# Performance work log

Measured on AMD Instinct MI355X. Metric: run time of the kernel, lower is better.

## Reference

```python
import jax, jax.numpy as jnp
import numpy as np

B, C, T_LEN, T_LAT = 32, 512, 1024, 31
T = T_LAT + 1          # t_len_block
NB = T_LEN // T        # n_blocks (t_pad == 0 by construction)
FS_SCALE = 10.0        # FastSigmoid surrogate scale

@jax.custom_vjp
def spike_fs(x):
    return (x > 0).astype(x.dtype)

def _fs_fwd(x):
    return (x > 0).astype(x.dtype), x

def _fs_bwd(x, g):
    return (g / (FS_SCALE * jnp.abs(x) + 1.0) ** 2,)

spike_fs.defvjp(_fs_fwd, _fs_bwd)

def _g(z):
    # keep entries exactly == 1, zero others; gradient passes through identically
    return z - jax.lax.stop_gradient(jnp.where(z == 1.0, 0.0, z))

def setup_inputs() -> dict:
    key = jax.random.key(0)
    k1, k2, k3, k4, k5 = jax.random.split(key, 5)
    x = jax.random.normal(k1, (B, C, T_LEN), jnp.float32)
    beta_raw = jax.random.uniform(k2, (C,), jnp.float32, 0.8, 0.95)   # _beta param
    rec_weight = jnp.eye(C, dtype=jnp.float32) + 0.05 * jax.random.normal(k3, (C, C), jnp.float32)
    p_raw = jax.random.uniform(k4, (C,), jnp.float32, 0.7, 0.95)      # _p param
    b_raw = jax.random.uniform(k5, (C,), jnp.float32, 0.3, 0.7)       # _b param
    return {"x": x, "beta_raw": beta_raw, "rec_weight": rec_weight, "p_raw": p_raw, "b_raw": b_raw}

def _forward(x, beta_raw, rec_weight, p_raw, b_raw):
    dt = x.dtype
    beta = jnp.clip(beta_raw, 0.001, 0.999)
    p = jnp.clip(jnp.abs(p_raw), 0.0, 0.999)
    b = jnp.clip(jnp.abs(b_raw), 0.001, 1.0)

    idx = jnp.arange(T)
    tril = idx[:, None] >= idx[None, :]
    # causal decay kernel: K[c,t,s] = beta_c**(t-s) for s<=t (== bconv1d with beta kernel)
    K = jnp.where(tril[None], beta[:, None, None] ** jnp.maximum(idx[:, None] - idx[None, :], 0).astype(dt), 0.0)
    # phi kernel: z[t] = sum_{s<=t} spikes[s] * (t-s+1)
    Zm = jnp.where(tril, (idx[:, None] - idx[None, :] + 1).astype(dt), 0.0)
    p_pow = p[:, None] ** jnp.arange(1, T + 1, dtype=dt)[None, :]  # (C,T)

    def block(cur, v_init, v_th):
        cur = cur.at[:, :, 0].add(beta[None, :] * v_init)
        mem = jnp.einsum('cts,bcs->bct', K, cur)          # (B,C,T)
        fs = spike_fs(mem - v_th)
        z = jnp.einsum('ts,bcs->bct', Zm, fs)
        return _g(z), z, mem

    Bx = x.shape[0]
    x_blocks = x.reshape(Bx, C, NB, T).transpose(2, 0, 1, 3)  # (NB,B,C,T)

    spikes0, z0, mem0 = block(x_blocks[0], jnp.zeros((Bx, C), dt), jnp.ones((Bx, C, T), dt))
    a_kernel0 = jnp.zeros((Bx, C, T), dt)

    def body(carry, x_slice):
        spikes_prev, z_prev, mem_last, a_kernel = carry
        sp_det = jax.lax.stop_gradient(spikes_prev)          # detach_spike_grad=True
        x_slice = x_slice + jnp.einsum('ij,bjt->bit', rec_weight, sp_det)
        mask_f = (jnp.max(sp_det, axis=2) != 0.0).astype(dt)  # (B,C) spike mask
        x_slice = jnp.where(z_prev < mask_f[:, :, None], 0.0, x_slice)  # refractory suppression
        v_init = mem_last * (1.0 - mask_f)
        # adaptation
        a_at_spike = jnp.sum(a_kernel * sp_det, axis=2) + 1.0 / p[None, :]
        decay_steps = jnp.sum((z_prev > 1.0).astype(dt), axis=2)
        new_a = a_at_spike * p[None, :] ** decay_steps
        a = a_kernel[:, :, -1] * (1.0 - mask_f) + new_a * mask_f
        a_kernel = p_pow[None] * a[:, :, None]               # (B,C,T)
        v_th = 1.0 + b[None, :, None] * a_kernel
        spikes, z, mem = block(x_slice, v_init, v_th)
        return (spikes, z, mem[:, :, -1], a_kernel), spikes

    carry0 = (spikes0, z0, mem0[:, :, -1], a_kernel0)
    _, spikes_rest = jax.lax.scan(body, carry0, x_blocks[1:])
    all_spikes = jnp.concatenate([spikes0[None], spikes_rest], axis=0)  # (NB,B,C,T)
    return all_spikes.transpose(1, 2, 0, 3).reshape(Bx, C, NB * T)

def reference(x, beta_raw, rec_weight, p_raw, b_raw):
    return _forward(x, beta_raw, rec_weight, p_raw, b_raw)
```

## Files before the change

### kernel.cpp

```cpp
#include <hip/hip_runtime.h>
#include <stdint.h>
#include <stddef.h>

#define CH     512
#define TT     32
#define NBLK   32
#define NBATCH 32
#define NCHUNK 8
#define NTHR   1024

__global__ __launch_bounds__(256) void transpose_k(const float* __restrict__ W,
                                                   float* __restrict__ WT) {
    __shared__ float tile[64][65];
    const int bx = blockIdx.x & 7, by = blockIdx.x >> 3;
    const int lx = threadIdx.x & 63, ly = threadIdx.x >> 6;
    for (int r = ly; r < 64; r += 4)
        tile[r][lx] = W[(size_t)(by * 64 + r) * CH + bx * 64 + lx];
    __syncthreads();
    for (int r = ly; r < 64; r += 4)
        WT[(size_t)(bx * 64 + r) * CH + by * 64 + lx] = tile[lx][r];
}

__global__ __launch_bounds__(NTHR, 4) void snn_kernel(
    const float* __restrict__ x,
    const float* __restrict__ beta_raw,
    const float* __restrict__ WT,
    const float* __restrict__ p_raw,
    const float* __restrict__ b_raw,
    int*       __restrict__ ent_g,
    float*     __restrict__ out)
{
    __shared__ float rec8[8][2112];
    __shared__ float rec_tot[2112];
    __shared__ int   ent_lds[512];
    __shared__ int   cnt_lds[8];
    __shared__ int   tf_lds[64];
    __shared__ int   tmp16[64];

    const int bidx = blockIdx.x;
    const int b    = bidx & (NBATCH - 1);
    const int kown = bidx >> 5;
    const int tid  = threadIdx.x;
    const int l    = tid & 63;
    const int g    = tid >> 6;
    const size_t base = ((size_t)b) << 19;
    int* pg = ent_g + (b << 8);

    const int c = (kown << 6) + l;
    const float beta  = fminf(fmaxf(beta_raw[c], 0.001f), 0.999f);
    const float p     = fminf(fabsf(p_raw[c]), 0.999f);
    const float bb    = fminf(fmaxf(fabsf(b_raw[c]), 0.001f), 1.0f);
    const float inv_p = 1.0f / p;
    float p32; { float t2 = p*p, t4 = t2*t2, t8 = t4*t4, t16 = t8*t8; p32 = t16*t16; }
    float a_mult = 0.f, v_init = 0.f;
    int   zero_start = 0;
    const unsigned long long lowmask = (1ull << l) - 1ull;

    if (tid < 512) {
        const int ch = tid >> 3, q = tid & 7;
        const float4 v = *(const float4*)(x + base + ((size_t)((kown << 6) + ch) << 10) + (q << 2));
        float* d = &rec8[0][ch * 33 + (q << 2)];
        d[0] = v.x; d[1] = v.y; d[2] = v.z; d[3] = v.w;
    } else {
        const int t0 = tid - 512;
        #pragma unroll
        for (int z = 0; z < 29; ++z) {
            const int k = t0 + (z << 9);
            if (k < 14784) (&rec8[1][0])[k] = 0.f;
        }
    }
    __syncthreads();

    for (int n = 0; n < NBLK; ++n) {
        int e0 = 0, e1 = 0, sp0 = 0, sp1 = 0;
        if (n > 0) {
            if (tid < 256) {
                const unsigned want = (unsigned)((n - 1) & 15);
                unsigned v;
                while (true) {
                    v = (unsigned)__hip_atomic_load(pg + tid, __ATOMIC_RELAXED, __HIP_MEMORY_SCOPE_AGENT);
                    if ((((v >> 12) & 15u) == want) && (((v >> 28) & 15u) == want)) break;
                    __builtin_amdgcn_s_sleep(1);
                }
                e0 = (int)(v & 0xFFFFu); e1 = (int)((v >> 16) & 0xFFFFu);
                sp0 = ((e0 >> 6) & 63) != 63;
                sp1 = ((e1 >> 6) & 63) != 63;
                const unsigned long long b0 = __ballot(sp0 != 0);
                const unsigned long long b1 = __ballot(sp1 != 0);
                if (l == 0) {
                    cnt_lds[(g << 1)]     = (int)__popcll(b0 & 0xFFFFFFFFull) + (int)__popcll(b1 & 0xFFFFFFFFull);
                    cnt_lds[(g << 1) | 1] = (int)__popcll(b0 >> 32) + (int)__popcll(b1 >> 32);
                }
            } else if (g == 8) {
                #pragma unroll
                for (int it = 0; it < 8; ++it) {
                    const int slot = (it << 6) + l;
                    const int ch = slot >> 3, q = slot & 7;
                    const int tf = tf_lds[ch];
                    const int t0 = q << 2;
                    float4 v;
                    v.x = (t0     == tf) ? 1.f : 0.f;
                    v.y = (t0 + 1 == tf) ? 1.f : 0.f;
                    v.z = (t0 + 2 == tf) ? 1.f : 0.f;
                    v.w = (t0 + 3 == tf) ? 1.f : 0.f;
                    *(float4*)(out + base + ((size_t)((kown << 6) + ch) << 10) + ((n - 1) << 5) + t0) = v;
                }
            }
        }
        __syncthreads();

        int L = 0;
        if (n > 0) {
            int pref = 0;
            const int mychunk = tid >> 5;
            #pragma unroll
            for (int k2 = 0; k2 < 8; ++k2) {
                const int ck = cnt_lds[k2];
                if (k2 < mychunk) pref += ck;
                L += ck;
            }
            if (tid < 256) {
                const int s0 = (tid & 31) << 1;
                const int chbase = (tid >> 5) << 6;
                if (sp0) ent_lds[pref + s0]     = ((chbase | (e0 & 63)) << 5) | ((e0 >> 6) & 31);
                if (sp1) ent_lds[pref + s0 + 1] = ((chbase | (e1 & 63)) << 5) | ((e1 >> 6) & 31);
            }
        }
        __syncthreads();

        float4 xstage;
        if (g >= 8) {
            if (n + 1 < NBLK) {
                const int slot = tid - 512;
                const int ch = slot >> 3, q = slot & 7;
                xstage = *(const float4*)(x + base + ((size_t)((kown << 6) + ch) << 10) + ((n + 1) << 5) + (q << 2));
            }
        } else if (L > 0) {
            const char* WTb = (const char*)WT;
            const int col4 = ((kown << 6) + l) << 2;
            float* myrec = &rec8[g][l * 33];
            float acc = 0.f; int cur_t = -1;
            #pragma unroll
            for (int s = 0; s < 8; ++s) {
                const int segbase = s << 6;
                if (segbase < L) {
                    const int ve = ent_lds[segbase + l];
                    int S[8]; float F[8];
                    #pragma unroll
                    for (int k = 0; k < 8; ++k) {
                        const int idx = segbase + g + (k << 3);
                        int sv = __builtin_amdgcn_readlane(ve, g + (k << 3));
                        const int ok = idx < L;
                        S[k] = ok ? sv : -1;
                        sv = ok ? sv : 0;
                        F[k] = *(const float*)(WTb + ((sv & 0xFFE0) << 6) + col4);
                    }
                    #pragma unroll
                    for (int k = 0; k < 8; ++k) {
                        if (S[k] >= 0) {
                            const int t = S[k] & 31;
                            if (t != cur_t) { if (cur_t >= 0) myrec[cur_t] += acc; acc = 0.f; cur_t = t; }
                            acc += F[k];
                        }
                    }
                }
            }
            if (cur_t >= 0) myrec[cur_t] += acc;
        }
        __syncthreads();

        #pragma unroll
        for (int r = 0; r < 2; ++r) {
            const int e = tid + (r << 10);
            const int idx = ((e >> 5) * 33) + (e & 31);
            rec_tot[idx] = ((rec8[0][idx] + rec8[1][idx]) + (rec8[2][idx] + rec8[3][idx]))
                         + ((rec8[4][idx] + rec8[5][idx]) + (rec8[6][idx] + rec8[7][idx]));
        }
        __syncthreads();

        if (g == 0) {
            float mem = 0.f, pc = p, pca = p;
            int t_first = -1;
            #pragma unroll
            for (int t = 0; t < TT; ++t) {
                const float rv = rec_tot[l * 33 + t];
                float cur = (t >= zero_start) ? rv : 0.f;
                if (t == 0) cur += beta * v_init;
                mem = beta * mem + cur;
                const float vth = 1.f + bb * pc * a_mult;
                if ((mem - vth > 0.f) && t_first < 0) { t_first = t; pca = pc; }
                pc *= p;
            }
            if (t_first >= 0) {
                float pd = 1.f;
                for (int m = 31 - t_first; m > 0; --m) pd *= p;
                a_mult = (pca * a_mult + inv_p) * pd;
                v_init = 0.f; zero_start = t_first;
            } else {
                a_mult = p32 * a_mult;
                v_init = mem; zero_start = 0;
            }
            tf_lds[l] = t_first;
            if (n + 1 < NBLK) {
                const bool sp = (t_first >= 0);
                const unsigned long long balS = __ballot(sp);
                const int cntS = (int)__popcll(balS);
                int mypos;
                if (sp) {
                    unsigned prefc = 0; int mp = 0;
                    #pragma unroll
                    for (int t = 0; t < TT; ++t) {
                        const unsigned long long bal = __ballot(t_first == t);
                        if (t_first == t) mp = (int)prefc + (int)__popcll(bal & lowmask);
                        prefc += (unsigned)__popcll(bal);
                    }
                    mypos = mp;
                } else {
                    mypos = cntS + (int)__popcll(~balS & lowmask);
                }
                const int tval = sp ? t_first : 63;
                tmp16[mypos] = ((n & 15) << 12) | (tval << 6) | l;
                __threadfence_block();
                if (l < 32) {
                    const int wlo = tmp16[l << 1];
                    const int whi = tmp16[(l << 1) | 1];
                    __hip_atomic_store(pg + (kown << 5) + l, wlo | (whi << 16),
                                       __ATOMIC_RELAXED, __HIP_MEMORY_SCOPE_AGENT);
                }
            }
        } else if (g >= 8) {
            if (n + 1 < NBLK) {
                const int slot = tid - 512;
                const int ch = slot >> 3, q = slot & 7;
                float* d = &rec8[0][ch * 33 + (q << 2)];
                d[0] = xstage.x; d[1] = xstage.y; d[2] = xstage.z; d[3] = xstage.w;
            }
        } else {
            if (n + 1 < NBLK) {
                const int t0 = tid - 64;
                #pragma unroll
                for (int z = 0; z < 33; ++z)
                    (&rec8[1][0])[t0 + 448 * z] = 0.f;
            }
        }
        __syncthreads();
    }

    if (tid < 512) {
        const int ch = tid >> 3, q = tid & 7;
        const int tf = tf_lds[ch];
        const int t0 = q << 2;
        float4 v;
        v.x = (t0     == tf) ? 1.f : 0.f;
        v.y = (t0 + 1 == tf) ? 1.f : 0.f;
        v.z = (t0 + 2 == tf) ? 1.f : 0.f;
        v.w = (t0 + 3 == tf) ? 1.f : 0.f;
        *(float4*)(out + base + ((size_t)((kown << 6) + ch) << 10) + (31 << 5) + t0) = v;
    }
}

extern "C" void kernel_launch(void* const* d_in, const int* in_sizes, int n_in,
                              void* d_out, int out_size, void* d_ws, size_t ws_size,
                              hipStream_t stream) {
    (void)in_sizes; (void)n_in; (void)out_size;
    const float* x   = (const float*)d_in[0];
    const float* br  = (const float*)d_in[1];
    const float* W   = (const float*)d_in[2];
    const float* pr  = (const float*)d_in[3];
    const float* bbr = (const float*)d_in[4];
    float* out = (float*)d_out;

    const size_t wt_bytes  = (size_t)CH * CH * sizeof(float);
    const size_t ent_bytes = (size_t)NBATCH * 256 * sizeof(int);
    if (ws_size < wt_bytes + ent_bytes) return;

    float* WT    = (float*)d_ws;
    int*   ent_g = (int*)((char*)d_ws + wt_bytes);

    transpose_k<<<64, 256, 0, stream>>>(W, WT);
    snn_kernel<<<NBATCH * NCHUNK, NTHR, 0, stream>>>(x, br, WT, pr, bbr, ent_g, out);
}
```

Measured before the change: 533.2 us.

## Remove two per-step barriers by having each wave poll and compact spike entries itself

Each compute wave now polls all 256 cross-block flag words itself and computes the spike counts and prefix offsets in registers. It writes its own compacted entry list, which removes the shared count array and two block-wide barriers per time block. The spike-output store and the next x prefetch move into the same phase on the upper waves. The firing-position ballot is folded into the membrane loop, replacing a separate 32-step ballot pass, and the scan wave gets raised scheduling priority. In exchange there is redundant polling and compaction across eight waves, plus more global atomic loads.

After: 521.4 us. -2.2%, faster.

```diff
diff --git a/kernel.cpp b/kernel.cpp
--- a/kernel.cpp
+++ b/kernel.cpp
@@ -32,8 +32,7 @@
 {
     __shared__ float rec8[8][2112];
     __shared__ float rec_tot[2112];
-    __shared__ int   ent_lds[512];
-    __shared__ int   cnt_lds[8];
+    __shared__ int   ent8[8][512];
     __shared__ int   tf_lds[64];
     __shared__ int   tmp16[64];
 
@@ -72,100 +71,123 @@
     __syncthreads();
 
     for (int n = 0; n < NBLK; ++n) {
-        int e0 = 0, e1 = 0, sp0 = 0, sp1 = 0;
-        if (n > 0) {
-            if (tid < 256) {
-                const unsigned want = (unsigned)((n - 1) & 15);
-                unsigned v;
+        float4 xstage;
+        if (g >= 8) {
+            const int slot = tid - 512;
+            const int ch = slot >> 3, q = slot & 7;
+            if (n + 1 < NBLK)
+                xstage = *(const float4*)(x + base + ((size_t)((kown << 6) + ch) << 10) + ((n + 1) << 5) + (q << 2));
+            if (n > 0) {
+                const int tf = tf_lds[ch];
+                const int t0 = q << 2;
+                float4 v;
+                v.x = (t0     == tf) ? 1.f : 0.f;
+                v.y = (t0 + 1 == tf) ? 1.f : 0.f;
+                v.z = (t0 + 2 == tf) ? 1.f : 0.f;
+                v.w = (t0 + 3 == tf) ? 1.f : 0.f;
+                *(float4*)(out + base + ((size_t)((kown << 6) + ch) << 10) + ((n - 1) << 5) + t0) = v;
+            }
+        } else if (n > 0) {
+            const unsigned want = (unsigned)((n - 1) & 15);
+            unsigned w0 = 0, w1 = 0, w2 = 0, w3 = 0;
+            {
+                bool d0 = false, d1 = false, d2 = false, d3 = false;
                 while (true) {
-                    v = (unsigned)__hip_atomic_load(pg + tid, __ATOMIC_RELAXED, __HIP_MEMORY_SCOPE_AGENT);
-                    if ((((v >> 12) & 15u) == want) && (((v >> 28) & 15u) == want)) break;
+#define TAGOK(v) (((((v) >> 12) & 15u) == want) && ((((v) >> 28) & 15u) == want))
+                    if (!d0) { const unsigned v = (unsigned)__hip_atomic_load(pg + l,       __ATOMIC_RELAXED, __HIP_MEMORY_SCOPE_AGENT); if (TAGOK(v)) { w0 = v; d0 = true; } }
+                    if (!d1) { const unsigned v = (unsigned)__hip_atomic_load(pg + 64 + l,  __ATOMIC_RELAXED, __HIP_MEMORY_SCOPE_AGENT); if (TAGOK(v)) { w1 = v; d1 = true; } }
+                    if (!d2) { const unsigned v = (unsigned)__hip_atomic_load(pg + 128 + l, __ATOMIC_RELAXED, __HIP_MEMORY_SCOPE_AGENT); if (TAGOK(v)) { w2 = v; d2 = true; } }
+                    if (!d3) { const unsigned v = (unsigned)__hip_atomic_load(pg + 192 + l, __ATOMIC_RELAXED, __HIP_MEMORY_SCOPE_AGENT); if (TAGOK(v)) { w3 = v; d3 = true; } }
+#undef TAGOK
+                    if (d0 && d1 && d2 && d3) break;
                     __builtin_amdgcn_s_sleep(1);
                 }
-                e0 = (int)(v & 0xFFFFu); e1 = (int)((v >> 16) & 0xFFFFu);
-                sp0 = ((e0 >> 6) & 63) != 63;
-                sp1 = ((e1 >> 6) & 63) != 63;
-                const unsigned long long b0 = __ballot(sp0 != 0);
-                const unsigned long long b1 = __ballot(sp1 != 0);
-                if (l == 0) {
-                    cnt_lds[(g << 1)]     = (int)__popcll(b0 & 0xFFFFFFFFull) + (int)__popcll(b1 & 0xFFFFFFFFull);
-                    cnt_lds[(g << 1) | 1] = (int)__popcll(b0 >> 32) + (int)__popcll(b1 >> 32);
-                }
-            } else if (g == 8) {
+            }
+            const unsigned long long LO32 = 0xFFFFFFFFull;
+            const int e00 = (int)(w0 & 0xFFFFu), e01 = (int)((w0 >> 16) & 0xFFFFu);
+            const int e10 = (int)(w1 & 0xFFFFu), e11 = (int)((w1 >> 16) & 0xFFFFu);
+            const int e20 = (int)(w2 & 0xFFFFu), e21 = (int)((w2 >> 16) & 0xFFFFu);
+            const int e30 = (int)(w3 & 0xFFFFu), e31 = (int)((w3 >> 16) & 0xFFFFu);
+            const int s00 = ((e00 >> 6) & 63) != 63, s01 = ((e01 >> 6) & 63) != 63;
+            const int s10 = ((e10 >> 6) & 63) != 63, s11 = ((e11 >> 6) & 63) != 63;
+            const int s20 = ((e20 >> 6) & 63) != 63, s21 = ((e21 >> 6) & 63) != 63;
+            const int s30 = ((e30 >> 6) & 63) != 63, s31 = ((e31 >> 6) & 63) != 63;
+            const unsigned long long b00 = __ballot(s00 != 0), b01 = __ballot(s01 != 0);
+            const unsigned long long b10 = __ballot(s10 != 0), b11 = __ballot(s11 != 0);
+            const unsigned long long b20 = __ballot(s20 != 0), b21 = __ballot(s21 != 0);
+            const unsigned long long b30 = __ballot(s30 != 0), b31 = __ballot(s31 != 0);
+            const int cnt0 = (int)__popcll(b00 & LO32) + (int)__popcll(b01 & LO32);
+            const int cnt1 = (int)__popcll(b00 >> 32)  + (int)__popcll(b01 >> 32);
+            const int cnt2 = (int)__popcll(b10 & LO32) + (int)__popcll(b11 & LO32);
+            const int cnt3 = (int)__popcll(b10 >> 32)  + (int)__popcll(b11 >> 32);
+            const int cnt4 = (int)__popcll(b20 & LO32) + (int)__popcll(b21 & LO32);
+            const int cnt5 = (int)__popcll(b20 >> 32)  + (int)__popcll(b21 >> 32);
+            const int cnt6 = (int)__popcll(b30 & LO32) + (int)__popcll(b31 & LO32);
+            const int cnt7 = (int)__popcll(b30 >> 32)  + (int)__popcll(b31 >> 32);
+            const int pf1 = cnt0;
+            const int pf2 = pf1 + cnt1;
+            const int pf3 = pf2 + cnt2;
+            const int pf4 = pf3 + cnt3;
+            const int pf5 = pf4 + cnt4;
+            const int pf6 = pf5 + cnt5;
+            const int pf7 = pf6 + cnt6;
+            const int L   = pf7 + cnt7;
+            const int hi = (l >> 5) & 1;
+            const int j2 = (l & 31) << 1;
+            int* entW = &ent8[g][0];
+            {
+                const int pc_ = hi ? pf1 : 0;    const int cb = (0 + hi) << 6;
+                if (s00) entW[pc_ + j2]     = ((cb | (e00 & 63)) << 5) | ((e00 >> 6) & 31);
+                if (s01) entW[pc_ + j2 + 1] = ((cb | (e01 & 63)) << 5) | ((e01 >> 6) & 31);
+            }
+            {
+                const int pc_ = hi ? pf3 : pf2;  const int cb = (2 + hi) << 6;
+                if (s10) entW[pc_ + j2]     = ((cb | (e10 & 63)) << 5) | ((e10 >> 6) & 31);
+                if (s11) entW[pc_ + j2 + 1] = ((cb | (e11 & 63)) << 5) | ((e11 >> 6) & 31);
+            }
+            {
+                const int pc_ = hi ? pf5 : pf4;  const int cb = (4 + hi) << 6;
+                if (s20) entW[pc_ + j2]     = ((cb | (e20 & 63)) << 5) | ((e20 >> 6) & 31);
+                if (s21) entW[pc_ + j2 + 1] = ((cb | (e21 & 63)) << 5) | ((e21 >> 6) & 31);
+            }
+            {
+                const int pc_ = hi ? pf7 : pf6;  const int cb = (6 + hi) << 6;
+                if (s30) entW[pc_ + j2]     = ((cb | (e30 & 63)) << 5) | ((e30 >> 6) & 31);
+                if (s31) entW[pc_ + j2 + 1] = ((cb | (e31 & 63)) << 5) | ((e31 >> 6) & 31);
+            }
+            __threadfence_block();
+            if (L > 0) {
+                const char* WTb = (const char*)WT;
+                const int col4 = ((kown << 6) + l) << 2;
+                float* myrec = &rec8[g][l * 33];
+                float acc = 0.f; int cur_t = -1;
                 #pragma unroll
-                for (int it = 0; it < 8; ++it) {
-                    const int slot = (it << 6) + l;
-                    const int ch = slot >> 3, q = slot & 7;
-                    const int tf = tf_lds[ch];
-                    const int t0 = q << 2;
-                    float4 v;
-                    v.x = (t0     == tf) ? 1.f : 0.f;
-                    v.y = (t0 + 1 == tf) ? 1.f : 0.f;
-                    v.z = (t0 + 2 == tf) ? 1.f : 0.f;
-                    v.w = (t0 + 3 == tf) ? 1.f : 0.f;
-                    *(float4*)(out + base + ((size_t)((kown << 6) + ch) << 10) + ((n - 1) << 5) + t0) = v;
-                }
-            }
-        }
-        __syncthreads();
-
-        int L = 0;
-        if (n > 0) {
-            int pref = 0;
-            const int mychunk = tid >> 5;
-            #pragma unroll
-            for (int k2 = 0; k2 < 8; ++k2) {
-                const int ck = cnt_lds[k2];
-                if (k2 < mychunk) pref += ck;
-                L += ck;
-            }
-            if (tid < 256) {
-                const int s0 = (tid & 31) << 1;
-                const int chbase = (tid >> 5) << 6;
-                if (sp0) ent_lds[pref + s0]     = ((chbase | (e0 & 63)) << 5) | ((e0 >> 6) & 31);
-                if (sp1) ent_lds[pref + s0 + 1] = ((chbase | (e1 & 63)) << 5) | ((e1 >> 6) & 31);
-            }
-        }
-        __syncthreads();
-
-        float4 xstage;
-        if (g >= 8) {
-            if (n + 1 < NBLK) {
-                const int slot = tid - 512;
-                const int ch = slot >> 3, q = slot & 7;
-                xstage = *(const float4*)(x + base + ((size_t)((kown << 6) + ch) << 10) + ((n + 1) << 5) + (q << 2));
-            }
-        } else if (L > 0) {
-            const char* WTb = (const char*)WT;
-            const int col4 = ((kown << 6) + l) << 2;
-            float* myrec = &rec8[g][l * 33];
-            float acc = 0.f; int cur_t = -1;
-            #pragma unroll
-            for (int s = 0; s < 8; ++s) {
-                const int segbase = s << 6;
-                if (segbase < L) {
-                    const int ve = ent_lds[segbase + l];
-                    int S[8]; float F[8];
-                    #pragma unroll
-                    for (int k = 0; k < 8; ++k) {
-                        const int idx = segbase + g + (k << 3);
-                        int sv = __builtin_amdgcn_readlane(ve, g + (k << 3));
-                        const int ok = idx < L;
-                        S[k] = ok ? sv : -1;
-                        sv = ok ? sv : 0;
-                        F[k] = *(const float*)(WTb + ((sv & 0xFFE0) << 6) + col4);
-                    }
-                    #pragma unroll
-                    for (int k = 0; k < 8; ++k) {
-                        if (S[k] >= 0) {
-                            const int t = S[k] & 31;
-                            if (t != cur_t) { if (cur_t >= 0) myrec[cur_t] += acc; acc = 0.f; cur_t = t; }
-                            acc += F[k];
+                for (int s = 0; s < 8; ++s) {
+                    const int segbase = s << 6;
+                    if (segbase < L) {
+                        const int ve = entW[segbase + l];
+                        int S[8]; float F[8];
+                        #pragma unroll
+                        for (int k = 0; k < 8; ++k) {
+                            const int idx = segbase + g + (k << 3);
+                            int sv = __builtin_amdgcn_readlane(ve, g + (k << 3));
+                            const int ok = idx < L;
+                            S[k] = ok ? sv : -1;
+                            sv = ok ? sv : 0;
+                            F[k] = *(const float*)(WTb + ((sv & 0xFFE0) << 6) + col4);
+                        }
+                        #pragma unroll
+                        for (int k = 0; k < 8; ++k) {
+                            if (S[k] >= 0) {
+                                const int t = S[k] & 31;
+                                if (t != cur_t) { if (cur_t >= 0) myrec[cur_t] += acc; acc = 0.f; cur_t = t; }
+                                acc += F[k];
+                            }
                         }
                     }
                 }
-            }
-            if (cur_t >= 0) myrec[cur_t] += acc;
+                if (cur_t >= 0) myrec[cur_t] += acc;
+            }
         }
         __syncthreads();
 
@@ -179,8 +201,10 @@
         __syncthreads();
 
         if (g == 0) {
+            __builtin_amdgcn_s_setprio(1);
             float mem = 0.f, pc = p, pca = p;
-            int t_first = -1;
+            int t_first = -1, mypos = 0;
+            unsigned prefc = 0;
             #pragma unroll
             for (int t = 0; t < TT; ++t) {
                 const float rv = rec_tot[l * 33 + t];
@@ -188,7 +212,13 @@
                 if (t == 0) cur += beta * v_init;
                 mem = beta * mem + cur;
                 const float vth = 1.f + bb * pc * a_mult;
-                if ((mem - vth > 0.f) && t_first < 0) { t_first = t; pca = pc; }
+                const bool fire = (mem - vth > 0.f) && (t_first < 0);
+                const unsigned long long bal = __ballot(fire);
+                if (fire) {
+                    t_first = t; pca = pc;
+                    mypos = (int)prefc + (int)__popcll(bal & lowmask);
+                }
+                prefc += (unsigned)__popcll(bal);
                 pc *= p;
             }
             if (t_first >= 0) {
@@ -204,20 +234,8 @@
             if (n + 1 < NBLK) {
                 const bool sp = (t_first >= 0);
                 const unsigned long long balS = __ballot(sp);
-                const int cntS = (int)__popcll(balS);
-                int mypos;
-                if (sp) {
-                    unsigned prefc = 0; int mp = 0;
-                    #pragma unroll
-                    for (int t = 0; t < TT; ++t) {
-                        const unsigned long long bal = __ballot(t_first == t);
-                        if (t_first == t) mp = (int)prefc + (int)__popcll(bal & lowmask);
-                        prefc += (unsigned)__popcll(bal);
-                    }
-                    mypos = mp;
-                } else {
-                    mypos = cntS + (int)__popcll(~balS & lowmask);
-                }
+                const int cntS = (int)prefc;
+                if (!sp) mypos = cntS + (int)__popcll(~balS & lowmask);
                 const int tval = sp ? t_first : 63;
                 tmp16[mypos] = ((n & 15) << 12) | (tval << 6) | l;
                 __threadfence_block();
@@ -228,6 +246,7 @@
                                        __ATOMIC_RELAXED, __HIP_MEMORY_SCOPE_AGENT);
                 }
             }
+            __builtin_amdgcn_s_setprio(0);
         } else if (g >= 8) {
             if (n + 1 < NBLK) {
                 const int slot = tid - 512;
```
